# Kernel tuning notes

Measured on AMD Instinct MI355X. Metric: run time of the kernel, lower is better.

The kernel has to match this reference:

```python
import jax, jax.numpy as jnp
import numpy as np

EPS = 1e-7        # Hyperboloid.eps for float32
MIN_NORM = 1e-15
MAX_NORM = 1e6
K = 1.0           # c = 1 -> K = 1/c
SQRT_K = 1.0
SLOPE = 0.01      # nn.LeakyReLU default negative_slope


def _cosh(x):
    return jnp.cosh(jnp.clip(x, -15.0, 15.0))


def _sinh(x):
    return jnp.sinh(jnp.clip(x, -15.0, 15.0))


def _arcosh(x):
    x = jnp.clip(x, 1.0 + 1e-7)
    return jnp.log(x + jnp.sqrt(x * x - 1.0))


def _norm(y):
    # safe row-norm (grad-finite at 0); original clamps norm to >=1e-15 anyway
    return jnp.sqrt(jnp.clip(jnp.sum(y * y, axis=-1, keepdims=True), 1e-30))


def mdot(x, y):
    return jnp.sum(x * y, axis=-1, keepdims=True) - 2.0 * x[..., :1] * y[..., :1]


def mnorm(u):
    return jnp.sqrt(jnp.clip(mdot(u, u), EPS))


def proj(x):
    y = x[..., 1:]
    x0 = jnp.sqrt(jnp.clip(K + jnp.sum(y * y, axis=-1, keepdims=True), EPS))
    return jnp.concatenate([x0, y], axis=-1)


def proj_tan0(u):
    return jnp.concatenate([jnp.zeros_like(u[..., :1]), u[..., 1:]], axis=-1)


def proj_tan(u, x):
    ux = jnp.sum(x[..., 1:] * u[..., 1:], axis=-1, keepdims=True)
    v0 = ux / jnp.clip(x[..., :1], EPS)
    return jnp.concatenate([v0, u[..., 1:]], axis=-1)


def expmap0(u):
    y = u[..., 1:]
    yn = jnp.clip(_norm(y), MIN_NORM)
    theta = yn / SQRT_K
    r0 = SQRT_K * _cosh(theta)
    r = SQRT_K * _sinh(theta) * y / yn
    return proj(jnp.concatenate([r0, r], axis=-1))


def logmap0(x):
    y = x[..., 1:]
    yn = jnp.clip(_norm(y), MIN_NORM)
    theta = jnp.clip(x[..., :1] / SQRT_K, 1.0 + EPS)
    r = SQRT_K * _arcosh(theta) * y / yn
    return jnp.concatenate([jnp.zeros_like(x[..., :1]), r], axis=-1)


def expmap(u, x):
    nu = jnp.clip(mnorm(u), None, MAX_NORM)
    theta = jnp.clip(nu / SQRT_K, MIN_NORM)
    return proj(_cosh(theta) * x + _sinh(theta) * u / theta)


def ptransp0(x, u):
    x0 = x[..., :1]
    y = x[..., 1:]
    yn = jnp.clip(_norm(y), MIN_NORM)
    y_hat = y / yn
    v = jnp.concatenate([-yn, (SQRT_K - x0) * y_hat], axis=-1)
    alpha = jnp.sum(y_hat * u[..., 1:], axis=-1, keepdims=True) / SQRT_K
    return proj_tan(u - alpha * v, x)


def mobius_add(x, y):
    u = logmap0(y)
    v = ptransp0(x, u)
    return expmap(v, x)


def hgcn_forward(x, adj, weight, bias):
    # map Euclidean input to the hyperboloid (HGCN.encode prologue)
    xh = proj(expmap0(proj_tan0(x)))
    # HypLinear: mobius_matvec (logmap0 -> matmul -> expmap0) + hyperbolic bias add
    res = proj(expmap0(logmap0(xh) @ weight.T))
    hyp_bias = proj(expmap0(proj_tan0(bias[None, :])))
    res = proj(mobius_add(res, hyp_bias))
    # HypAgg (use_att=False): aggregate in tangent space at origin via spmm
    h = proj(expmap0(adj @ logmap0(res)))
    # HypAct: LeakyReLU in tangent space, then back to hyperboloid
    t = proj_tan0(jax.nn.leaky_relu(logmap0(h), SLOPE))
    return proj(expmap0(t))


def setup_inputs() -> dict:
    key = jax.random.key(0)
    k1, k2, k3, k4 = jax.random.split(key, 4)
    N, D = 8192, 64
    x = jax.random.normal(k1, (N, D), dtype=jnp.float32)
    adj = jax.random.uniform(k2, (N, N), dtype=jnp.float32)
    adj = adj / jnp.sum(adj, axis=1, keepdims=True)  # row-normalized dense adjacency
    weight = jax.random.uniform(k3, (D, D), dtype=jnp.float32)  # init.uniform_ in [0,1)
    bias = 0.01 * jax.random.normal(k4, (D,), dtype=jnp.float32)
    return {"x": x, "adj": adj, "weight": weight, "bias": bias}


def reference(x, adj, weight, bias):
    return hgcn_forward(x, adj, weight, bias)
```

## Files before the change

### kernel.cpp

```cpp
#include <hip/hip_runtime.h>
#include <hip/hip_bf16.h>
#include <math.h>

typedef __bf16 bf16x8 __attribute__((ext_vector_type(8)));
typedef __bf16 bf16x4 __attribute__((ext_vector_type(4)));
typedef float  f32x4  __attribute__((ext_vector_type(4)));

#define NND 8192
#define DIM 64
#define PB  10368

__device__ __forceinline__ float wsum(float v) {
#pragma unroll
    for (int m = 1; m < 64; m <<= 1) v += __shfl_xor(v, m, 64);
    return v;
}

struct SC { float sh, ch; };
__device__ __forceinline__ SC sinhcosh(float c) {
    float e  = expf(c);
    float ei = 1.0f / e;
    SC r; r.sh = 0.5f * (e - ei); r.ch = 0.5f * (e + ei);
    return r;
}

__device__ __forceinline__ float arcosh_from_n2(float n2) {
    float t = fmaxf(n2, 2.0000001e-7f);
    return logf(sqrtf(1.0f + t) + sqrtf(t));
}

__device__ __forceinline__ float tangent_chain(float xv, int lane) {
    float y   = (lane == 0) ? 0.0f : xv;
    float yn2 = wsum(y * y);
    float yn  = fmaxf(sqrtf(fmaxf(yn2, 1e-30f)), 1e-15f);
    SC s1 = sinhcosh(fminf(yn, 15.0f));
    float r   = (lane == 0) ? 0.0f : s1.sh * y / yn;
    float rn2 = wsum(r * r);
    float ynb = fmaxf(sqrtf(fmaxf(rn2, 1e-30f)), 1e-15f);
    float ac  = arcosh_from_n2(rn2);
    return (lane == 0) ? 0.0f : ac * r / ynb;
}

__device__ __forceinline__ float second_chain(float m, float ubv, float theta_b, int lane) {
    float my  = (lane == 0) ? 0.0f : m;
    float mn2 = wsum(my * my);
    float mn  = fmaxf(sqrtf(fmaxf(mn2, 1e-30f)), 1e-15f);
    SC s2 = sinhcosh(fminf(mn, 15.0f));
    float rr   = (lane == 0) ? 0.0f : s2.sh * my / mn;
    float rrn2 = wsum(rr * rr);
    float res0 = sqrtf(fmaxf(1.0f + rrn2, 1e-7f));
    float yn3   = fmaxf(sqrtf(fmaxf(rrn2, 1e-30f)), 1e-15f);
    float yhat  = (lane == 0) ? 0.0f : rr / yn3;
    float alpha = wsum(yhat * ubv);
    float w_    = ubv - alpha * (1.0f - res0) * yhat;
    float ux    = wsum(rr * w_);
    float v0    = ux / fmaxf(res0, 1e-7f);
    float vv    = (lane == 0) ? v0 : w_;
    float resv  = (lane == 0) ? res0 : rr;
    float theta = theta_b;
    SC s3 = sinhcosh(fminf(theta, 15.0f));
    float pv  = s3.ch * resv + s3.sh * vv / theta;
    float pn2 = wsum((lane == 0) ? 0.0f : pv * pv);
    float yn4 = fmaxf(sqrtf(fmaxf(pn2, 1e-30f)), 1e-15f);
    float ac4 = arcosh_from_n2(pn2);
    return (lane == 0) ? 0.0f : ac4 * pv / yn4;
}

__device__ __forceinline__ float epilogue_chain(float hv, int lane) {
    float y   = (lane == 0) ? 0.0f : hv;
    float yn2 = wsum(y * y);
    float yn  = fmaxf(sqrtf(fmaxf(yn2, 1e-30f)), 1e-15f);
    SC s1 = sinhcosh(fminf(yn, 15.0f));
    float r   = (lane == 0) ? 0.0f : s1.sh * y / yn;
    float rn2 = wsum(r * r);
    float ynb = fmaxf(sqrtf(fmaxf(rn2, 1e-30f)), 1e-15f);
    float ac  = arcosh_from_n2(rn2);
    float lgv = (lane == 0) ? 0.0f : ac * r / ynb;
    float t   = (lgv > 0.0f) ? lgv : 0.01f * lgv;
    float tn2 = wsum(t * t);
    float tn  = fmaxf(sqrtf(fmaxf(tn2, 1e-30f)), 1e-15f);
    SC s3 = sinhcosh(fminf(tn, 15.0f));
    float ov  = (lane == 0) ? 0.0f : s3.sh * t / tn;
    float on2 = wsum(ov * ov);
    float o0  = sqrtf(fmaxf(1.0f + on2, 1e-7f));
    return (lane == 0) ? o0 : ov;
}

__global__ __launch_bounds__(256) void k_prep(
    const float* __restrict__ x, const float* __restrict__ weight,
    const float* __restrict__ bias, __bf16* __restrict__ l2bf)
{
    __shared__ float WL[64][65];
    const int tid  = threadIdx.x;
    const int lane = tid & 63;
    const int wave = tid >> 6;
#pragma unroll
    for (int i = 0; i < 16; ++i) {
        int idx = i * 256 + tid;
        WL[idx >> 6][idx & 63] = weight[idx];
    }
    __syncthreads();
    float ubv  = tangent_chain(bias[lane], lane);
    float nub2 = wsum(ubv * ubv);
    float thb  = fmaxf(fminf(sqrtf(fmaxf(nub2, 1e-7f)), 1e6f), 1e-15f);

    const int row = blockIdx.x * 4 + wave;
    float xv  = x[row * 64 + lane];
    float L1v = tangent_chain(xv, lane);
    float mj0 = 0.f, mj1 = 0.f, mj2 = 0.f, mj3 = 0.f;
#pragma unroll
    for (int d = 0; d < 64; d += 4) {
        mj0 = fmaf(__shfl(L1v, d,     64), WL[lane][d],     mj0);
        mj1 = fmaf(__shfl(L1v, d + 1, 64), WL[lane][d + 1], mj1);
        mj2 = fmaf(__shfl(L1v, d + 2, 64), WL[lane][d + 2], mj2);
        mj3 = fmaf(__shfl(L1v, d + 3, 64), WL[lane][d + 3], mj3);
    }
    float mj  = (mj0 + mj1) + (mj2 + mj3);
    float L2v = second_chain(mj, ubv, thb, lane);
    l2bf[(size_t)lane * PB + row] = (__bf16)L2v;
}

#define ISSUE_A(T, V)  V = *reinterpret_cast<const f32x4*>(gA + (T) * 64);
#define WRITE_A(T, V)  do {                                                     \
    bf16x4 p_; p_[0]=(__bf16)V[0]; p_[1]=(__bf16)V[1];                          \
    p_[2]=(__bf16)V[2]; p_[3]=(__bf16)V[3];                                     \
    *reinterpret_cast<bf16x4*>(As[(T) & 1] + aw_idx) = p_;                      \
} while (0)
#define COMPUTE(T) do {                                                         \
    _Pragma("unroll")                                                           \
    for (int s_ = 0; s_ < 2; ++s_) {                                            \
        bf16x8 a_ = *reinterpret_cast<const bf16x8*>(                           \
            As[(T) & 1] + ar_row * 64 + (((4 * s_ + lg) ^ lx7) * 8));           \
        bf16x8 b_ = *reinterpret_cast<const bf16x8*>(                           \
            Bs + br_row * 256 + (((((T) & 3) * 8 + 4 * s_ + lg) ^ lx7) * 8));   \
        acc = __builtin_amdgcn_mfma_f32_16x16x32_bf16(a_, b_, acc, 0, 0, 0);    \
    }                                                                           \
} while (0)
#define STAGE_B(Q) do {                                                         \
    _Pragma("unroll")                                                           \
    for (int i_ = 0; i_ < 4; ++i_) {                                            \
        const int f_ = i_ * 512 + tid;                                          \
        const int r_ = f_ >> 5, c_ = f_ & 31;                                   \
        vb[i_] = *reinterpret_cast<const bf16x8*>(                              \
            l2bf + (size_t)r_ * PB + kc + (Q) * 256 + c_ * 8);                  \
    }                                                                           \
} while (0)
#define WRITE_B() do {                                                          \
    _Pragma("unroll")                                                           \
    for (int i_ = 0; i_ < 4; ++i_) {                                            \
        const int f_ = i_ * 512 + tid;                                          \
        const int r_ = f_ >> 5, c_ = f_ & 31;                                   \
        *reinterpret_cast<bf16x8*>(Bs + r_ * 256 + ((c_ ^ (r_ & 7)) * 8)) = vb[i_]; \
    }                                                                           \
} while (0)

__global__ __launch_bounds__(512, 6) void k_mm(
    const float* __restrict__ adj, const __bf16* __restrict__ l2bf,
    float* __restrict__ pws)
{
    __shared__ __bf16 Bs[64 * 256];
    __shared__ __bf16 As[2][32 * 64];
    const int tid  = threadIdx.x;
    const int lane = tid & 63;
    const int w    = tid >> 6;
    const int l15  = lane & 15;
    const int lg   = lane >> 4;
    const int lx7  = l15 & 7;
    const int rh   = w >> 2;
    const int dq   = w & 3;
    const int rg   = blockIdx.x & 255;
    const int kch  = blockIdx.x >> 8;
    const int R0   = rg * 32;
    const int kc   = kch * 1024;

    const int arow = tid >> 4;
    const int acol = (tid & 15) * 4;
    const int aw_idx = arow * 64 + (((acol >> 3) ^ (arow & 7)) * 8) + (acol & 7);
    const int ar_row = rh * 16 + l15;
    const int br_row = dq * 16 + l15;
    const float* gA = adj + (size_t)(R0 + arow) * NND + kc + acol;

    f32x4 va0, va1, va2, va3;
    bf16x8 vb[4];
    f32x4 acc = {0.f, 0.f, 0.f, 0.f};

    STAGE_B(0);
    ISSUE_A(0, va0); ISSUE_A(1, va1); ISSUE_A(2, va2); ISSUE_A(3, va3);
    WRITE_B();
    WRITE_A(0, va0);
    ISSUE_A(4, va0);
    __syncthreads();

    COMPUTE(0);                WRITE_A(1, va1);  ISSUE_A(5, va1);  __syncthreads();
    COMPUTE(1);  STAGE_B(1);   WRITE_A(2, va2);  ISSUE_A(6, va2);  __syncthreads();
    COMPUTE(2);                WRITE_A(3, va3);  ISSUE_A(7, va3);  __syncthreads();
    COMPUTE(3);  __syncthreads();  WRITE_B();
                               WRITE_A(4, va0);  ISSUE_A(8, va0);  __syncthreads();
    COMPUTE(4);                WRITE_A(5, va1);  ISSUE_A(9, va1);  __syncthreads();
    COMPUTE(5);  STAGE_B(2);   WRITE_A(6, va2);  ISSUE_A(10, va2); __syncthreads();
    COMPUTE(6);                WRITE_A(7, va3);  ISSUE_A(11, va3); __syncthreads();
    COMPUTE(7);  __syncthreads();  WRITE_B();
                               WRITE_A(8, va0);  ISSUE_A(12, va0); __syncthreads();
    COMPUTE(8);                WRITE_A(9, va1);  ISSUE_A(13, va1); __syncthreads();
    COMPUTE(9);  STAGE_B(3);   WRITE_A(10, va2); ISSUE_A(14, va2); __syncthreads();
    COMPUTE(10);               WRITE_A(11, va3); ISSUE_A(15, va3); __syncthreads();
    COMPUTE(11); __syncthreads();  WRITE_B();
                               WRITE_A(12, va0);                   __syncthreads();
    COMPUTE(12);               WRITE_A(13, va1);                   __syncthreads();
    COMPUTE(13);               WRITE_A(14, va2);                   __syncthreads();
    COMPUTE(14);               WRITE_A(15, va3);                   __syncthreads();
    COMPUTE(15);

    float* pp = pws + (size_t)kch * NND * DIM;
#pragma unroll
    for (int i = 0; i < 4; ++i) {
        pp[(size_t)(R0 + rh * 16 + lg * 4 + i) * DIM + dq * 16 + l15] = acc[i];
    }
}

__global__ __launch_bounds__(256) void k_fin(
    const float* __restrict__ pws, float* __restrict__ out)
{
    const int tid  = threadIdx.x;
    const int lane = tid & 63;
    const int wave = tid >> 6;
    const int row  = blockIdx.x * 4 + wave;
    const size_t base = (size_t)row * DIM + lane;
    const size_t S = (size_t)NND * DIM;
    float hv = (((pws[base] + pws[S + base]) + (pws[2*S + base] + pws[3*S + base]))
             +  ((pws[4*S + base] + pws[5*S + base]) + (pws[6*S + base] + pws[7*S + base])));
    out[base] = epilogue_chain(hv, lane);
}

extern "C" void kernel_launch(void* const* d_in, const int* in_sizes, int n_in,
                              void* d_out, int out_size, void* d_ws, size_t ws_size,
                              hipStream_t stream)
{
    const float* x      = (const float*)d_in[0];
    const float* adj    = (const float*)d_in[1];
    const float* weight = (const float*)d_in[2];
    const float* bias   = (const float*)d_in[3];
    float* out = (float*)d_out;
    __bf16* l2bf = (__bf16*)d_ws;
    float*  pws  = (float*)((char*)d_ws + 0x180000);

    k_prep<<<2048, 256, 0, stream>>>(x, weight, bias, l2bf);
    k_mm<<<2048, 512, 0, stream>>>(adj, l2bf, pws);
    k_fin<<<2048, 256, 0, stream>>>(pws, out);
}
```

Measured before the change: 79.95 us.

## Double row tile per block to reuse staged B across 64 adjacency rows

Each k_mm block now covers 64 adjacency rows instead of 32, and each wave computes two 16x16 output tiles that share one A fragment. The grid is halved to 1024 blocks. The staged l2bf (B) tile is therefore loaded once per 64 rows, halving global and LDS staging traffic for B per output row. The A prefetch depth drops from 4 to 3 buffers, each now holding two rows, which raises register use. Fewer blocks and a bigger As array may reduce occupancy and latency hiding on the bandwidth-bound adj stream.

```diff
diff --git a/kernel.cpp b/kernel.cpp
--- a/kernel.cpp
+++ b/kernel.cpp
@@ -120,20 +120,28 @@
     l2bf[(size_t)lane * PB + row] = (__bf16)L2v;
 }
 
-#define ISSUE_A(T, V)  V = *reinterpret_cast<const f32x4*>(gA + (T) * 64);
-#define WRITE_A(T, V)  do {                                                     \
-    bf16x4 p_; p_[0]=(__bf16)V[0]; p_[1]=(__bf16)V[1];                          \
-    p_[2]=(__bf16)V[2]; p_[3]=(__bf16)V[3];                                     \
+#define ISSUE_A(T, V, W) do {                                                   \
+    V = *reinterpret_cast<const f32x4*>(gA  + (T) * 64);                        \
+    W = *reinterpret_cast<const f32x4*>(gA2 + (T) * 64);                        \
+} while (0)
+#define WRITE_A(T, V, W) do {                                                   \
+    bf16x4 p_, q_;                                                              \
+    p_[0]=(__bf16)V[0]; p_[1]=(__bf16)V[1]; p_[2]=(__bf16)V[2]; p_[3]=(__bf16)V[3]; \
+    q_[0]=(__bf16)W[0]; q_[1]=(__bf16)W[1]; q_[2]=(__bf16)W[2]; q_[3]=(__bf16)W[3]; \
     *reinterpret_cast<bf16x4*>(As[(T) & 1] + aw_idx) = p_;                      \
+    *reinterpret_cast<bf16x4*>(As[(T) & 1] + aw_idx + 32 * 64) = q_;            \
 } while (0)
 #define COMPUTE(T) do {                                                         \
     _Pragma("unroll")                                                           \
     for (int s_ = 0; s_ < 2; ++s_) {                                            \
-        bf16x8 a_ = *reinterpret_cast<const bf16x8*>(                           \
+        bf16x8 a_  = *reinterpret_cast<const bf16x8*>(                          \
             As[(T) & 1] + ar_row * 64 + (((4 * s_ + lg) ^ lx7) * 8));           \
-        bf16x8 b_ = *reinterpret_cast<const bf16x8*>(                           \
-            Bs + br_row * 256 + (((((T) & 3) * 8 + 4 * s_ + lg) ^ lx7) * 8));   \
-        acc = __builtin_amdgcn_mfma_f32_16x16x32_bf16(a_, b_, acc, 0, 0, 0);    \
+        bf16x8 b0_ = *reinterpret_cast<const bf16x8*>(                          \
+            Bs + br0 * 256 + (((((T) & 3) * 8 + 4 * s_ + lg) ^ lx7) * 8));      \
+        bf16x8 b1_ = *reinterpret_cast<const bf16x8*>(                          \
+            Bs + br1 * 256 + (((((T) & 3) * 8 + 4 * s_ + lg) ^ lx7) * 8));      \
+        acc0 = __builtin_amdgcn_mfma_f32_16x16x32_bf16(a_, b0_, acc0, 0, 0, 0); \
+        acc1 = __builtin_amdgcn_mfma_f32_16x16x32_bf16(a_, b1_, acc1, 0, 0, 0); \
     }                                                                           \
 } while (0)
 #define STAGE_B(Q) do {                                                         \
@@ -159,62 +167,67 @@
     float* __restrict__ pws)
 {
     __shared__ __bf16 Bs[64 * 256];
-    __shared__ __bf16 As[2][32 * 64];
+    __shared__ __bf16 As[2][64 * 64];
     const int tid  = threadIdx.x;
     const int lane = tid & 63;
     const int w    = tid >> 6;
     const int l15  = lane & 15;
     const int lg   = lane >> 4;
     const int lx7  = l15 & 7;
-    const int rh   = w >> 2;
-    const int dq   = w & 3;
-    const int rg   = blockIdx.x & 255;
-    const int kch  = blockIdx.x >> 8;
-    const int R0   = rg * 32;
+    const int rq   = w >> 1;
+    const int dh   = w & 1;
+    const int rg   = blockIdx.x & 127;
+    const int kch  = blockIdx.x >> 7;
+    const int R0   = rg * 64;
     const int kc   = kch * 1024;
 
     const int arow = tid >> 4;
     const int acol = (tid & 15) * 4;
     const int aw_idx = arow * 64 + (((acol >> 3) ^ (arow & 7)) * 8) + (acol & 7);
-    const int ar_row = rh * 16 + l15;
-    const int br_row = dq * 16 + l15;
-    const float* gA = adj + (size_t)(R0 + arow) * NND + kc + acol;
-
-    f32x4 va0, va1, va2, va3;
+    const int ar_row = rq * 16 + l15;
+    const int br0 = dh * 32 + l15;
+    const int br1 = dh * 32 + 16 + l15;
+    const float* gA  = adj + (size_t)(R0 + arow) * NND + kc + acol;
+    const float* gA2 = gA + (size_t)32 * NND;
+
+    f32x4 va0, va0b, va1, va1b, va2, va2b;
     bf16x8 vb[4];
-    f32x4 acc = {0.f, 0.f, 0.f, 0.f};
+    f32x4 acc0 = {0.f, 0.f, 0.f, 0.f};
+    f32x4 acc1 = acc0;
 
     STAGE_B(0);
-    ISSUE_A(0, va0); ISSUE_A(1, va1); ISSUE_A(2, va2); ISSUE_A(3, va3);
+    ISSUE_A(0, va0, va0b); ISSUE_A(1, va1, va1b); ISSUE_A(2, va2, va2b);
     WRITE_B();
-    WRITE_A(0, va0);
-    ISSUE_A(4, va0);
+    WRITE_A(0, va0, va0b);
+    ISSUE_A(3, va0, va0b);
     __syncthreads();
 
-    COMPUTE(0);                WRITE_A(1, va1);  ISSUE_A(5, va1);  __syncthreads();
-    COMPUTE(1);  STAGE_B(1);   WRITE_A(2, va2);  ISSUE_A(6, va2);  __syncthreads();
-    COMPUTE(2);                WRITE_A(3, va3);  ISSUE_A(7, va3);  __syncthreads();
+    COMPUTE(0);                WRITE_A(1, va1, va1b);  ISSUE_A(4, va1, va1b);  __syncthreads();
+    COMPUTE(1);  STAGE_B(1);   WRITE_A(2, va2, va2b);  ISSUE_A(5, va2, va2b);  __syncthreads();
+    COMPUTE(2);                WRITE_A(3, va0, va0b);  ISSUE_A(6, va0, va0b);  __syncthreads();
     COMPUTE(3);  __syncthreads();  WRITE_B();
-                               WRITE_A(4, va0);  ISSUE_A(8, va0);  __syncthreads();
-    COMPUTE(4);                WRITE_A(5, va1);  ISSUE_A(9, va1);  __syncthreads();
-    COMPUTE(5);  STAGE_B(2);   WRITE_A(6, va2);  ISSUE_A(10, va2); __syncthreads();
-    COMPUTE(6);                WRITE_A(7, va3);  ISSUE_A(11, va3); __syncthreads();
+                               WRITE_A(4, va1, va1b);  ISSUE_A(7, va1, va1b);  __syncthreads();
+    COMPUTE(4);                WRITE_A(5, va2, va2b);  ISSUE_A(8, va2, va2b);  __syncthreads();
+    COMPUTE(5);  STAGE_B(2);   WRITE_A(6, va0, va0b);  ISSUE_A(9, va0, va0b);  __syncthreads();
+    COMPUTE(6);                WRITE_A(7, va1, va1b);  ISSUE_A(10, va1, va1b); __syncthreads();
     COMPUTE(7);  __syncthreads();  WRITE_B();
-                               WRITE_A(8, va0);  ISSUE_A(12, va0); __syncthreads();
-    COMPUTE(8);                WRITE_A(9, va1);  ISSUE_A(13, va1); __syncthreads();
-    COMPUTE(9);  STAGE_B(3);   WRITE_A(10, va2); ISSUE_A(14, va2); __syncthreads();
-    COMPUTE(10);               WRITE_A(11, va3); ISSUE_A(15, va3); __syncthreads();
+                               WRITE_A(8, va2, va2b);  ISSUE_A(11, va2, va2b); __syncthreads();
+    COMPUTE(8);                WRITE_A(9, va0, va0b);  ISSUE_A(12, va0, va0b); __syncthreads();
+    COMPUTE(9);  STAGE_B(3);   WRITE_A(10, va1, va1b); ISSUE_A(13, va1, va1b); __syncthreads();
+    COMPUTE(10);               WRITE_A(11, va2, va2b); ISSUE_A(14, va2, va2b); __syncthreads();
     COMPUTE(11); __syncthreads();  WRITE_B();
-                               WRITE_A(12, va0);                   __syncthreads();
-    COMPUTE(12);               WRITE_A(13, va1);                   __syncthreads();
-    COMPUTE(13);               WRITE_A(14, va2);                   __syncthreads();
-    COMPUTE(14);               WRITE_A(15, va3);                   __syncthreads();
+                               WRITE_A(12, va0, va0b); ISSUE_A(15, va0, va0b); __syncthreads();
+    COMPUTE(12);               WRITE_A(13, va1, va1b);                         __syncthreads();
+    COMPUTE(13);               WRITE_A(14, va2, va2b);                         __syncthreads();
+    COMPUTE(14);               WRITE_A(15, va0, va0b);                         __syncthreads();
     COMPUTE(15);
 
     float* pp = pws + (size_t)kch * NND * DIM;
 #pragma unroll
     for (int i = 0; i < 4; ++i) {
-        pp[(size_t)(R0 + rh * 16 + lg * 4 + i) * DIM + dq * 16 + l15] = acc[i];
+        const size_t grow = (size_t)(R0 + rq * 16 + lg * 4 + i);
+        pp[grow * DIM + dh * 32 + l15]      = acc0[i];
+        pp[grow * DIM + dh * 32 + 16 + l15] = acc1[i];
     }
 }
 
@@ -245,6 +258,6 @@
     float*  pws  = (float*)((char*)d_ws + 0x180000);
 
     k_prep<<<2048, 256, 0, stream>>>(x, weight, bias, l2bf);
-    k_mm<<<2048, 512, 0, stream>>>(adj, l2bf, pws);
+    k_mm<<<1024, 512, 0, stream>>>(adj, l2bf, pws);
     k_fin<<<2048, 256, 0, stream>>>(pws, out);
 }
```

Result: slower. 132.0 us (+65.1%).
